# Kernel optimization log

Hardware: AMD Instinct MI355X
Metric: run time of the kernel (lower is better)

## Reference

```python
import jax, jax.numpy as jnp
import numpy as np

N = 50000   # nodes
E = 800000  # edges
G = 64      # graphs in batch
EPS = 1e-5  # BatchNorm eps


def setup_inputs() -> dict:
    key = jax.random.key(0)
    ks = jax.random.split(key, 32)
    inp = {
        'x': jax.random.normal(ks[0], (N, 1), jnp.float32),
        'edge_index': jax.random.randint(ks[1], (2, E), 0, N),
        'batch': jnp.sort(jax.random.randint(ks[2], (N,), 0, G)),
    }
    dims = [(1, 64), (64, 64), (64, 64), (64, 64)]
    for i, (din, dout) in enumerate(dims, 1):
        inp[f'W{i}'] = jax.random.normal(ks[2 + i], (din, dout), jnp.float32) / np.sqrt(din)
        inp[f'b{i}'] = jnp.zeros((dout,), jnp.float32)
        inp[f'g{i}'] = jnp.ones((dout,), jnp.float32)
        inp[f'bt{i}'] = jnp.zeros((dout,), jnp.float32)
    inp['fw1'] = jax.random.normal(ks[10], (128, 64), jnp.float32) / 8.0
    inp['fb1'] = jnp.zeros((128,), jnp.float32)
    inp['fw2'] = jax.random.normal(ks[11], (10, 128), jnp.float32) / np.sqrt(128)
    inp['fb2'] = jnp.zeros((10,), jnp.float32)
    return inp


def _gcn_norm(edge_index):
    # add self-loops, symmetric normalization (PyG GCNConv default)
    loop = jnp.arange(N)
    row = jnp.concatenate([edge_index[0], loop])
    col = jnp.concatenate([edge_index[1], loop])
    deg = jax.ops.segment_sum(jnp.ones_like(col, jnp.float32), col, num_segments=N)
    dinv = jnp.where(deg > 0, deg ** -0.5, 0.0)
    norm = dinv[row] * dinv[col]
    return row, col, norm


def _gcn(x, W, b, row, col, norm):
    h = x @ W                                   # [N, dout]
    msg = h[row] * norm[:, None]                # gather + scale per edge
    agg = jax.ops.segment_sum(msg, col, num_segments=N)  # scatter-add
    return agg + b


def _bn(x, g, bt):
    m = x.mean(0)
    v = x.var(0)
    return g * (x - m) * jax.lax.rsqrt(v + EPS) + bt


def reference(x, edge_index, batch,
              W1, b1, g1, bt1, W2, b2, g2, bt2,
              W3, b3, g3, bt3, W4, b4, g4, bt4,
              fw1, fb1, fw2, fb2):
    row, col, norm = _gcn_norm(edge_index)
    x = jax.nn.relu(_bn(_gcn(x, W1, b1, row, col, norm), g1, bt1))
    x = jax.nn.relu(_bn(_gcn(x, W2, b2, row, col, norm), g2, bt2))
    x = jax.nn.relu(_bn(_gcn(x, W3, b3, row, col, norm), g3, bt3))
    x = jax.nn.relu(_bn(_gcn(x, W4, b4, row, col, norm), g4, bt4))
    # global mean pool over graphs
    cnt = jax.ops.segment_sum(jnp.ones((N,), jnp.float32), batch, num_segments=G)
    pooled = jax.ops.segment_sum(x, batch, num_segments=G) / jnp.clip(cnt, 1.0)[:, None]
    h = jax.nn.relu(pooled @ fw1.T + fb1)
    return h @ fw2.T + fb2
```

## Files before the change

kernel.cpp:

```cpp
#include <hip/hip_runtime.h>

#define NN 50000
#define NE 800000
#define NG 64
#define FD 64
#define BN_EPS 1e-5f
#define SCAN_B 256
#define NBIN 98
#define BINCAP 12288
#define SCH 4096
#define SCH_NBLK ((NE + SCH - 1) / SCH)
#define INV_NN (1.0f / NN)
#define MM_NBLK ((NN + 3) / 4)

__global__ __launch_bounds__(256) void k_binscatter(const int* __restrict__ row,
                                                    const int* __restrict__ col,
                                                    int* __restrict__ gcnt,
                                                    int* __restrict__ bins) {
    __shared__ int stage[SCH];
    __shared__ int cnt[NBIN], off[NBIN + 1], cur[NBIN], gbase[NBIN];
    int t = threadIdx.x;
    int e0 = blockIdx.x * SCH;
    int nk = NE - e0; if (nk > SCH) nk = SCH;
    if (nk <= 0) return;
    for (int b = t; b < NBIN; b += 256) cnt[b] = 0;
    __syncthreads();
    for (int k = t; k < nk; k += 256) {
        int c = col[e0 + k];
        atomicAdd(&cnt[c >> 9], 1);
    }
    __syncthreads();
    if (t == 0) {
        int run = 0;
        for (int b = 0; b < NBIN; ++b) { off[b] = run; run += cnt[b]; }
        off[NBIN] = run;
    }
    __syncthreads();
    if (t < NBIN) {
        cur[t] = off[t];
        gbase[t] = t * BINCAP + atomicAdd(&gcnt[t], cnt[t]);
    }
    __syncthreads();
    for (int k = t; k < nk; k += 256) {
        int c = col[e0 + k];
        int r = row[e0 + k];
        int b = c >> 9;
        int pos = atomicAdd(&cur[b], 1);
        stage[pos] = ((c & 511) << 16) | r;
    }
    __syncthreads();
    for (int k = t; k < nk; k += 256) {
        int lo = 0, hi = NBIN - 1;
        while (lo < hi) {
            int mid = (lo + hi + 1) >> 1;
            if (off[mid] <= k) lo = mid; else hi = mid - 1;
        }
        bins[gbase[lo] + (k - off[lo])] = stage[k];
    }
}

__global__ __launch_bounds__(256) void k_binscan(const int* __restrict__ gcnt,
                                                 const int* __restrict__ bins,
                                                 const float* __restrict__ x,
                                                 int* __restrict__ cursor,
                                                 int* __restrict__ bsum,
                                                 float* __restrict__ dinv,
                                                 float* __restrict__ xd) {
    __shared__ int ldeg[512];
    __shared__ int psc[256];
    int b = blockIdx.x, t = threadIdx.x;
    for (int l = t; l < 512; l += 256) ldeg[l] = 0;
    __syncthreads();
    int nb = gcnt[b];
    const int* bp = bins + b * BINCAP;
    for (int k = t; k < nb; k += 256) atomicAdd(&ldeg[bp[k] >> 16], 1);
    __syncthreads();
    int d0 = ldeg[2 * t], d1 = ldeg[2 * t + 1];
    int pv = d0 + d1;
    psc[t] = pv;
    __syncthreads();
    for (int off = 1; off < 256; off <<= 1) {
        int u = (t >= off) ? psc[t - off] : 0;
        __syncthreads();
        psc[t] += u;
        __syncthreads();
    }
    int excl = psc[t] - pv;
    int base = b << 9;
    int i0 = base + 2 * t, i1 = i0 + 1;
    if (i0 < NN) {
        cursor[i0] = excl;
        float dv = rsqrtf((float)d0 + 1.0f);
        dinv[i0] = dv; xd[i0] = x[i0] * dv;
    }
    if (i1 < NN) {
        cursor[i1] = excl + d0;
        float dv = rsqrtf((float)d1 + 1.0f);
        dinv[i1] = dv; xd[i1] = x[i1] * dv;
    }
    if (t == 255) bsum[b] = psc[255];
}

__global__ __launch_bounds__(SCAN_B) void k_scan_top(int* __restrict__ bsum,
                                                     float* __restrict__ stats) {
    __shared__ int sh[SCAN_B];
    int t = threadIdx.x;
    if (t < 2) stats[t] = 0.0f;
    int v = (t < NBIN) ? bsum[t] : 0;
    sh[t] = v;
    __syncthreads();
    for (int off = 1; off < SCAN_B; off <<= 1) {
        int u = (t >= off) ? sh[t - off] : 0;
        __syncthreads();
        sh[t] += u;
        __syncthreads();
    }
    if (t < NBIN) bsum[t] = sh[t] - v;
}

__global__ __launch_bounds__(256) void k_binfill_l1(const int* __restrict__ gcnt,
                                                    const int* __restrict__ bins,
                                                    const int* __restrict__ cursor,
                                                    const int* __restrict__ bsum,
                                                    int* __restrict__ eidx,
                                                    const float* __restrict__ xd,
                                                    const float* __restrict__ x,
                                                    const float* __restrict__ dinv,
                                                    float* __restrict__ s,
                                                    float* __restrict__ stats) {
    __shared__ int lstart[512], lcur[512];
    __shared__ float ls[256], lq[256];
    int b = blockIdx.x, t = threadIdx.x;
    int base = b << 9;
    int bofs = bsum[b];
    for (int l = t; l < 512; l += 256) {
        int i = base + l;
        int st = (i < NN) ? cursor[i] + bofs : 0;
        lstart[l] = st; lcur[l] = st;
    }
    __syncthreads();
    int nb = gcnt[b];
    const int* bp = bins + b * BINCAP;
    for (int k = t; k < nb; k += 256) {
        int v = bp[k];
        int pos = atomicAdd(&lcur[v >> 16], 1);
        eidx[pos] = v & 0xFFFF;
    }
    __syncthreads();
    float a = 0.0f, q = 0.0f;
    #pragma unroll
    for (int half = 0; half < 2; ++half) {
        int l = t + half * 256;
        int i = base + l;
        if (i < NN) {
            float acc = 0.0f;
            int e0 = lstart[l], e1 = lcur[l];
            for (int k = e0; k < e1; ++k) acc += xd[eidx[k]];
            float di = dinv[i];
            float sv = di * (acc + di * x[i]);
            s[i] = sv;
            a += sv; q += sv * sv;
        }
    }
    ls[t] = a; lq[t] = q;
    __syncthreads();
    for (int st = 128; st > 0; st >>= 1) {
        if (t < st) { ls[t] += ls[t + st]; lq[t] += lq[t + st]; }
        __syncthreads();
    }
    if (t == 0) { atomicAdd(&stats[0], ls[0]); atomicAdd(&stats[1], lq[0]); }
}

__global__ __launch_bounds__(256) void k_mm_l1(const float* __restrict__ s,
                                               const float* __restrict__ stats,
                                               const float* __restrict__ W1,
                                               const float* __restrict__ g1,
                                               const float* __restrict__ bt1,
                                               const float* __restrict__ W,
                                               float* __restrict__ h) {
    __shared__ float Ws[64 * 64];
    __shared__ float xs[4 * 64];
    __shared__ float als[64], cls[64];
    int t = threadIdx.x;
    for (int k = t; k < 64 * 64; k += 256) Ws[k] = W[k];
    if (t < 64) {
        float mean = stats[0] * INV_NN;
        float var  = stats[1] * INV_NN - mean * mean;
        float w = W1[t];
        float rinv = rsqrtf(var * w * w + BN_EPS);
        float a = g1[t] * w * rinv;
        als[t] = a;
        cls[t] = bt1[t] - a * mean;
    }
    __syncthreads();
    int n0 = blockIdx.x * 4;
    int j = t & 63, n = t >> 6;
    int node = n0 + n;
    float sv = (node < NN) ? s[node] : 0.0f;
    xs[t] = fmaxf(als[j] * sv + cls[j], 0.0f);
    __syncthreads();
    if (node < NN) {
        float acc = 0.f;
        #pragma unroll
        for (int k = 0; k < 64; ++k) acc += xs[n * 64 + k] * Ws[k * 64 + j];
        h[node * 64 + j] = acc;
    }
}

__global__ __launch_bounds__(256) void k_mm_bn(const float* __restrict__ src,
                                               const float* __restrict__ bnsum,
                                               const float* __restrict__ bnsq,
                                               const float* __restrict__ g,
                                               const float* __restrict__ bt,
                                               const float* __restrict__ W,
                                               float* __restrict__ h) {
    __shared__ float Ws[64 * 64];
    __shared__ float xs[4 * 64];
    __shared__ float scl[64], shf[64];
    int t = threadIdx.x;
    for (int k = t; k < 64 * 64; k += 256) Ws[k] = W[k];
    if (t < 64) {
        float mean = bnsum[t] * INV_NN;
        float var  = bnsq[t] * INV_NN - mean * mean;
        float rinv = rsqrtf(var + BN_EPS);
        float sc = g[t] * rinv;
        scl[t] = sc;
        shf[t] = bt[t] - sc * mean;
    }
    __syncthreads();
    int n0 = blockIdx.x * 4;
    int j = t & 63, n = t >> 6;
    int node = n0 + n;
    int gidx = n0 * 64 + t;
    float v = (gidx < NN * 64) ? src[gidx] : 0.0f;
    xs[t] = fmaxf(scl[j] * v + shf[j], 0.0f);
    __syncthreads();
    if (node < NN) {
        float acc = 0.f;
        #pragma unroll
        for (int k = 0; k < 64; ++k) acc += xs[n * 64 + k] * Ws[k * 64 + j];
        h[node * 64 + j] = acc;
    }
}

__global__ __launch_bounds__(256) void k_gather(const int* __restrict__ cursor,
                                                const int* __restrict__ bsum,
                                                const int* __restrict__ eidx,
                                                const float* __restrict__ dinv,
                                                const float* __restrict__ h,
                                                const float* __restrict__ b,
                                                float* __restrict__ agg,
                                                float* __restrict__ bnsumz,
                                                float* __restrict__ bnsqz) {
    if (blockIdx.x == 0) {
        int t = threadIdx.x;
        if (t < 64) bnsumz[t] = 0.0f;
        else if (t < 128) bnsqz[t - 64] = 0.0f;
    }
    int node = blockIdx.x * 4 + (threadIdx.x >> 6);
    if (node >= NN) return;
    int lane = threadIdx.x & 63;
    int eslot = lane >> 4;
    int fb = (lane & 15) << 2;
    int start = cursor[node] + bsum[node >> 9];
    int end = (node < NN - 1) ? cursor[node + 1] + bsum[(node + 1) >> 9] : NE;
    float4 acc0 = make_float4(0.f, 0.f, 0.f, 0.f);
    float4 acc1 = make_float4(0.f, 0.f, 0.f, 0.f);
    int e = start + eslot;
    for (; e + 4 < end; e += 8) {
        int r0 = eidx[e], r1 = eidx[e + 4];
        float dr0 = dinv[r0], dr1 = dinv[r1];
        const float4 h0 = *reinterpret_cast<const float4*>(&h[r0 * 64 + fb]);
        const float4 h1 = *reinterpret_cast<const float4*>(&h[r1 * 64 + fb]);
        acc0.x += h0.x * dr0; acc0.y += h0.y * dr0; acc0.z += h0.z * dr0; acc0.w += h0.w * dr0;
        acc1.x += h1.x * dr1; acc1.y += h1.y * dr1; acc1.z += h1.z * dr1; acc1.w += h1.w * dr1;
    }
    if (e < end) {
        int r = eidx[e];
        float dr = dinv[r];
        const float4 hv = *reinterpret_cast<const float4*>(&h[r * 64 + fb]);
        acc0.x += hv.x * dr; acc0.y += hv.y * dr; acc0.z += hv.z * dr; acc0.w += hv.w * dr;
    }
    acc0.x += acc1.x; acc0.y += acc1.y; acc0.z += acc1.z; acc0.w += acc1.w;
    acc0.x += __shfl_xor(acc0.x, 16); acc0.y += __shfl_xor(acc0.y, 16);
    acc0.z += __shfl_xor(acc0.z, 16); acc0.w += __shfl_xor(acc0.w, 16);
    acc0.x += __shfl_xor(acc0.x, 32); acc0.y += __shfl_xor(acc0.y, 32);
    acc0.z += __shfl_xor(acc0.z, 32); acc0.w += __shfl_xor(acc0.w, 32);
    if (lane < 16) {
        float dc = dinv[node];
        const float4 hv = *reinterpret_cast<const float4*>(&h[node * 64 + fb]);
        const float4 bv = *reinterpret_cast<const float4*>(&b[fb]);
        float4 o;
        o.x = dc * (acc0.x + dc * hv.x) + bv.x;
        o.y = dc * (acc0.y + dc * hv.y) + bv.y;
        o.z = dc * (acc0.z + dc * hv.z) + bv.z;
        o.w = dc * (acc0.w + dc * hv.w) + bv.w;
        *reinterpret_cast<float4*>(&agg[node * 64 + fb]) = o;
    }
}

__global__ __launch_bounds__(256) void k_bn_stats(const float* __restrict__ agg,
                                                  float* __restrict__ bnsum, float* __restrict__ bnsq,
                                                  float* __restrict__ pooledz, float* __restrict__ cntz) {
    if (pooledz != nullptr && blockIdx.x == 0) {
        for (int k = threadIdx.x; k < 64 * 64; k += 256) pooledz[k] = 0.0f;
        if (threadIdx.x < 64) cntz[threadIdx.x] = 0.0f;
    }
    __shared__ float ls[256], lq[256];
    int j = threadIdx.x & 63, nl = threadIdx.x >> 6;
    float a = 0.f, b = 0.f;
    for (int i = blockIdx.x * 4 + nl; i < NN; i += gridDim.x * 4) {
        float v = agg[i * 64 + j]; a += v; b += v * v;
    }
    ls[threadIdx.x] = a; lq[threadIdx.x] = b; __syncthreads();
    if (threadIdx.x < 128) { ls[threadIdx.x] += ls[threadIdx.x + 128]; lq[threadIdx.x] += lq[threadIdx.x + 128]; }
    __syncthreads();
    if (threadIdx.x < 64) {
        atomicAdd(&bnsum[j], ls[threadIdx.x] + ls[threadIdx.x + 64]);
        atomicAdd(&bnsq[j],  lq[threadIdx.x] + lq[threadIdx.x + 64]);
    }
}

__global__ __launch_bounds__(256) void k_pool_bn(const float* __restrict__ agg,
                                                 const float* __restrict__ bnsum,
                                                 const float* __restrict__ bnsq,
                                                 const float* __restrict__ g4,
                                                 const float* __restrict__ bt4,
                                                 const int* __restrict__ batch,
                                                 float* __restrict__ pooled,
                                                 float* __restrict__ cnt) {
    const int wpb = 4;
    int wave = blockIdx.x * wpb + (threadIdx.x >> 6);
    int lane = threadIdx.x & 63;
    const int nwaves = gridDim.x * wpb;
    int chunk = (NN + nwaves - 1) / nwaves;
    int i0 = wave * chunk;
    int i1 = i0 + chunk; if (i1 > NN) i1 = NN;
    if (i0 >= NN) return;
    float mean = bnsum[lane] * INV_NN;
    float var  = bnsq[lane] * INV_NN - mean * mean;
    float rinv = rsqrtf(var + BN_EPS);
    float sc = g4[lane] * rinv;
    float sh = bt4[lane] - sc * mean;
    float acc = 0.0f;
    int curb = batch[i0];
    int runlen = 0;
    for (int i = i0; i < i1; ++i) {
        int b = batch[i];
        if (b != curb) {
            atomicAdd(&pooled[curb * 64 + lane], acc);
            if (lane == 0) atomicAdd(&cnt[curb], (float)runlen);
            acc = 0.0f; runlen = 0; curb = b;
        }
        acc += fmaxf(sc * agg[i * 64 + lane] + sh, 0.0f);
        ++runlen;
    }
    atomicAdd(&pooled[curb * 64 + lane], acc);
    if (lane == 0) atomicAdd(&cnt[curb], (float)runlen);
}

__global__ __launch_bounds__(128) void k_fc(const float* __restrict__ pooled, const float* __restrict__ cnt,
                                            const float* __restrict__ fw1, const float* __restrict__ fb1,
                                            const float* __restrict__ fw2, const float* __restrict__ fb2,
                                            float* __restrict__ out) {
    __shared__ float p[64], hsh[128];
    int g = blockIdx.x, t = threadIdx.x;
    if (t < 64) {
        float c = cnt[g]; c = c < 1.f ? 1.f : c;
        p[t] = pooled[g * 64 + t] / c;
    }
    __syncthreads();
    float acc = fb1[t];
    #pragma unroll 8
    for (int k = 0; k < 64; ++k) acc += p[k] * fw1[t * 64 + k];
    hsh[t] = fmaxf(acc, 0.f);
    __syncthreads();
    if (t < 10) {
        float o = fb2[t];
        #pragma unroll 8
        for (int k = 0; k < 128; ++k) o += hsh[k] * fw2[t * 128 + k];
        out[g * 10 + t] = o;
    }
}

extern "C" void kernel_launch(void* const* d_in, const int* in_sizes, int n_in,
                              void* d_out, int out_size, void* d_ws, size_t ws_size,
                              hipStream_t stream) {
    const float* x   = (const float*)d_in[0];
    const int* ei    = (const int*)d_in[1];
    const int* batch = (const int*)d_in[2];
    const float* W[5]  = {nullptr, (const float*)d_in[3],  (const float*)d_in[7],
                                   (const float*)d_in[11], (const float*)d_in[15]};
    const float* bb[5] = {nullptr, (const float*)d_in[4],  (const float*)d_in[8],
                                   (const float*)d_in[12], (const float*)d_in[16]};
    const float* gg[5] = {nullptr, (const float*)d_in[5],  (const float*)d_in[9],
                                   (const float*)d_in[13], (const float*)d_in[17]};
    const float* bt[5] = {nullptr, (const float*)d_in[6],  (const float*)d_in[10],
                                   (const float*)d_in[14], (const float*)d_in[18]};
    const float* fw1 = (const float*)d_in[19];
    const float* fb1 = (const float*)d_in[20];
    const float* fw2 = (const float*)d_in[21];
    const float* fb2 = (const float*)d_in[22];
    float* out = (float*)d_out;

    const int* row = ei;
    const int* col = ei + NE;

    float* ws = (float*)d_ws;
    int*   cursor  = (int*)ws;
    int*   eidx    = (int*)(ws + 50000);
    float* dinv    = ws + 850000;
    float* xd      = ws + 900000;
    int*   bsum    = (int*)(ws + 950000);
    float* s       = ws + 951000;
    float* stats   = ws + 1001008;
    float* bnsum   = ws + 1001072;
    float* bnsq    = ws + 1001136;
    float* pooled  = ws + 1001360;
    float* cnt     = ws + 1005456;
    int*   gcnt    = (int*)(ws + 1056000);
    float* hbuf    = ws + 1100000;
    int*   bins    = (int*)(ws + 1100000);
    float* aggbuf  = ws + 4300000;

    const int B = 256;

    hipMemsetAsync(gcnt, 0, NBIN * sizeof(int), stream);
    k_binscatter<<<SCH_NBLK, B, 0, stream>>>(row, col, gcnt, bins);
    k_binscan<<<NBIN, B, 0, stream>>>(gcnt, bins, x, cursor, bsum, dinv, xd);
    k_scan_top<<<1, SCAN_B, 0, stream>>>(bsum, stats);
    k_binfill_l1<<<NBIN, B, 0, stream>>>(gcnt, bins, cursor, bsum, eidx, xd, x, dinv, s, stats);

    k_mm_l1<<<MM_NBLK, B, 0, stream>>>(s, stats, W[1], gg[1], bt[1], W[2], hbuf);
    k_gather<<<MM_NBLK, B, 0, stream>>>(cursor, bsum, eidx, dinv, hbuf, bb[2], aggbuf, bnsum, bnsq);
    k_bn_stats<<<512, B, 0, stream>>>(aggbuf, bnsum, bnsq, nullptr, nullptr);

    for (int L = 3; L <= 4; ++L) {
        k_mm_bn<<<MM_NBLK, B, 0, stream>>>(aggbuf, bnsum, bnsq, gg[L - 1], bt[L - 1], W[L], hbuf);
        k_gather<<<MM_NBLK, B, 0, stream>>>(cursor, bsum, eidx, dinv, hbuf, bb[L], aggbuf, bnsum, bnsq);
        k_bn_stats<<<512, B, 0, stream>>>(aggbuf, bnsum, bnsq,
                                          (L == 4) ? pooled : nullptr, (L == 4) ? cnt : nullptr);
    }

    k_pool_bn<<<512, B, 0, stream>>>(aggbuf, bnsum, bnsq, gg[4], bt[4], batch, pooled, cnt);
    k_fc<<<NG, 128, 0, stream>>>(pooled, cnt, fw1, fb1, fw2, fb2, out);
}
```

Baseline: 335.2 us.

## Store transformed features in fp16 for gather and replace binary search with stored bin ids

The per-layer feature matrix h written by the matmul kernels is now stored as half precision, and the gather kernel loads 8-byte half4 vectors and widens them to float. This halves the bytes moved in the edge-gather pass, which is bound by irregular memory reads. Separately, the bin-scatter kernel records each staged edge's bin id in a byte array, so the write-out loop no longer needs a binary search over the bin offsets. The fp16 storage adds rounding error to the features before aggregation, which may loosen the match against the fp32 reference.

```diff
diff --git a/kernel.cpp b/kernel.cpp
--- a/kernel.cpp
+++ b/kernel.cpp
@@ -1,4 +1,5 @@
 #include <hip/hip_runtime.h>
+#include <hip/hip_fp16.h>
 
 #define NN 50000
 #define NE 800000
@@ -18,7 +19,8 @@
                                                     int* __restrict__ gcnt,
                                                     int* __restrict__ bins) {
     __shared__ int stage[SCH];
-    __shared__ int cnt[NBIN], off[NBIN + 1], cur[NBIN], gbase[NBIN];
+    __shared__ unsigned char stageb[SCH];
+    __shared__ int cnt[NBIN], off[NBIN], cur[NBIN], gbase[NBIN];
     int t = threadIdx.x;
     int e0 = blockIdx.x * SCH;
     int nk = NE - e0; if (nk > SCH) nk = SCH;
@@ -33,7 +35,6 @@
     if (t == 0) {
         int run = 0;
         for (int b = 0; b < NBIN; ++b) { off[b] = run; run += cnt[b]; }
-        off[NBIN] = run;
     }
     __syncthreads();
     if (t < NBIN) {
@@ -47,15 +48,12 @@
         int b = c >> 9;
         int pos = atomicAdd(&cur[b], 1);
         stage[pos] = ((c & 511) << 16) | r;
+        stageb[pos] = (unsigned char)b;
     }
     __syncthreads();
     for (int k = t; k < nk; k += 256) {
-        int lo = 0, hi = NBIN - 1;
-        while (lo < hi) {
-            int mid = (lo + hi + 1) >> 1;
-            if (off[mid] <= k) lo = mid; else hi = mid - 1;
-        }
-        bins[gbase[lo] + (k - off[lo])] = stage[k];
+        int b = stageb[k];
+        bins[gbase[b] + (k - off[b])] = stage[k];
     }
 }
 
@@ -177,7 +175,7 @@
                                                const float* __restrict__ g1,
                                                const float* __restrict__ bt1,
                                                const float* __restrict__ W,
-                                               float* __restrict__ h) {
+                                               __half* __restrict__ h) {
     __shared__ float Ws[64 * 64];
     __shared__ float xs[4 * 64];
     __shared__ float als[64], cls[64];
@@ -203,7 +201,7 @@
         float acc = 0.f;
         #pragma unroll
         for (int k = 0; k < 64; ++k) acc += xs[n * 64 + k] * Ws[k * 64 + j];
-        h[node * 64 + j] = acc;
+        h[node * 64 + j] = __float2half(acc);
     }
 }
 
@@ -213,7 +211,7 @@
                                                const float* __restrict__ g,
                                                const float* __restrict__ bt,
                                                const float* __restrict__ W,
-                                               float* __restrict__ h) {
+                                               __half* __restrict__ h) {
     __shared__ float Ws[64 * 64];
     __shared__ float xs[4 * 64];
     __shared__ float scl[64], shf[64];
@@ -239,7 +237,7 @@
         float acc = 0.f;
         #pragma unroll
         for (int k = 0; k < 64; ++k) acc += xs[n * 64 + k] * Ws[k * 64 + j];
-        h[node * 64 + j] = acc;
+        h[node * 64 + j] = __float2half(acc);
     }
 }
 
@@ -247,7 +245,7 @@
                                                 const int* __restrict__ bsum,
                                                 const int* __restrict__ eidx,
                                                 const float* __restrict__ dinv,
-                                                const float* __restrict__ h,
+                                                const __half* __restrict__ h,
                                                 const float* __restrict__ b,
                                                 float* __restrict__ agg,
                                                 float* __restrict__ bnsumz,
@@ -270,16 +268,22 @@
     for (; e + 4 < end; e += 8) {
         int r0 = eidx[e], r1 = eidx[e + 4];
         float dr0 = dinv[r0], dr1 = dinv[r1];
-        const float4 h0 = *reinterpret_cast<const float4*>(&h[r0 * 64 + fb]);
-        const float4 h1 = *reinterpret_cast<const float4*>(&h[r1 * 64 + fb]);
-        acc0.x += h0.x * dr0; acc0.y += h0.y * dr0; acc0.z += h0.z * dr0; acc0.w += h0.w * dr0;
-        acc1.x += h1.x * dr1; acc1.y += h1.y * dr1; acc1.z += h1.z * dr1; acc1.w += h1.w * dr1;
+        uint2 u0 = *reinterpret_cast<const uint2*>(&h[r0 * 64 + fb]);
+        uint2 u1 = *reinterpret_cast<const uint2*>(&h[r1 * 64 + fb]);
+        float2 a01 = __half22float2(*reinterpret_cast<__half2*>(&u0.x));
+        float2 a23 = __half22float2(*reinterpret_cast<__half2*>(&u0.y));
+        float2 b01 = __half22float2(*reinterpret_cast<__half2*>(&u1.x));
+        float2 b23 = __half22float2(*reinterpret_cast<__half2*>(&u1.y));
+        acc0.x += a01.x * dr0; acc0.y += a01.y * dr0; acc0.z += a23.x * dr0; acc0.w += a23.y * dr0;
+        acc1.x += b01.x * dr1; acc1.y += b01.y * dr1; acc1.z += b23.x * dr1; acc1.w += b23.y * dr1;
     }
     if (e < end) {
         int r = eidx[e];
         float dr = dinv[r];
-        const float4 hv = *reinterpret_cast<const float4*>(&h[r * 64 + fb]);
-        acc0.x += hv.x * dr; acc0.y += hv.y * dr; acc0.z += hv.z * dr; acc0.w += hv.w * dr;
+        uint2 u0 = *reinterpret_cast<const uint2*>(&h[r * 64 + fb]);
+        float2 a01 = __half22float2(*reinterpret_cast<__half2*>(&u0.x));
+        float2 a23 = __half22float2(*reinterpret_cast<__half2*>(&u0.y));
+        acc0.x += a01.x * dr; acc0.y += a01.y * dr; acc0.z += a23.x * dr; acc0.w += a23.y * dr;
     }
     acc0.x += acc1.x; acc0.y += acc1.y; acc0.z += acc1.z; acc0.w += acc1.w;
     acc0.x += __shfl_xor(acc0.x, 16); acc0.y += __shfl_xor(acc0.y, 16);
@@ -288,13 +292,15 @@
     acc0.z += __shfl_xor(acc0.z, 32); acc0.w += __shfl_xor(acc0.w, 32);
     if (lane < 16) {
         float dc = dinv[node];
-        const float4 hv = *reinterpret_cast<const float4*>(&h[node * 64 + fb]);
+        uint2 u0 = *reinterpret_cast<const uint2*>(&h[node * 64 + fb]);
+        float2 s01 = __half22float2(*reinterpret_cast<__half2*>(&u0.x));
+        float2 s23 = __half22float2(*reinterpret_cast<__half2*>(&u0.y));
         const float4 bv = *reinterpret_cast<const float4*>(&b[fb]);
         float4 o;
-        o.x = dc * (acc0.x + dc * hv.x) + bv.x;
-        o.y = dc * (acc0.y + dc * hv.y) + bv.y;
-        o.z = dc * (acc0.z + dc * hv.z) + bv.z;
-        o.w = dc * (acc0.w + dc * hv.w) + bv.w;
+        o.x = dc * (acc0.x + dc * s01.x) + bv.x;
+        o.y = dc * (acc0.y + dc * s01.y) + bv.y;
+        o.z = dc * (acc0.z + dc * s23.x) + bv.z;
+        o.w = dc * (acc0.w + dc * s23.y) + bv.w;
         *reinterpret_cast<float4*>(&agg[node * 64 + fb]) = o;
     }
 }
@@ -419,7 +425,7 @@
     float* pooled  = ws + 1001360;
     float* cnt     = ws + 1005456;
     int*   gcnt    = (int*)(ws + 1056000);
-    float* hbuf    = ws + 1100000;
+    __half* hbuf   = (__half*)(ws + 1100000);
     int*   bins    = (int*)(ws + 1100000);
     float* aggbuf  = ws + 4300000;
 
```

After: 322.9 us. 1.04x faster.
